# Optimization experiments

Measured on AMD Instinct MI355X. Metric: run time of the kernel, lower is better.

Reference implementation:

```python
import jax, jax.numpy as jnp
import numpy as np

N = 262144      # total atoms (ragged over batch)
B = 64          # batch_size
K = 16          # retrieved features per sample
H = 256         # h_dim
R = 512         # ret_feat_dim


def setup_inputs() -> dict:
    key = jax.random.key(0)
    k1, k2, k3, k4, k5, k6, k7 = jax.random.split(key, 7)
    h = jax.random.normal(k1, (N, H), dtype=jnp.float32)
    ret_feat = jax.random.normal(k2, (B, K, R), dtype=jnp.float32)
    batch = jnp.sort(jax.random.randint(k3, (N,), 0, B, dtype=jnp.int64))
    # nn.Linear weights: y = x @ W.T + b
    Wp = jax.random.normal(k4, (H, R), dtype=jnp.float32) / np.sqrt(R)
    bp = jax.random.normal(k5, (H,), dtype=jnp.float32) * 0.01
    Wl = jax.random.normal(k6, (H, 2 * H), dtype=jnp.float32) / np.sqrt(2 * H)
    bl = jax.random.normal(k7, (H,), dtype=jnp.float32) * 0.01
    return {"h": h, "ret_feat": ret_feat, "batch": batch,
            "Wp": Wp, "bp": bp, "Wl": Wl, "bl": bl}


def reference(h, ret_feat, batch, Wp, bp, Wl, bl):
    # ret_feat: [B, K, R] -> mean over K -> project to [B, H]
    ret = jnp.mean(ret_feat, axis=1)                    # [B, R]
    ret = ret @ Wp.T + bp                               # [B, H]
    # The torch loop gathers h[batch==i], concats the pooled feature
    # repeated per atom, applies `linear`, and scatters back. Since every
    # atom is covered exactly once, this is a per-node gather + linear:
    per_node = ret[batch]                               # [N, H] gather
    x = jnp.concatenate([h, per_node], axis=-1)         # [N, 2H]
    return x @ Wl.T + bl                                # [N, H]
```

## Files before the change

kernel.cpp:

```cpp
#include <hip/hip_runtime.h>
#include <hip/hip_bf16.h>

#define N_ATOMS 262144
#define B_SZ    64
#define H_DIM   256
#define R_DIM   512

#define TILE_ROWS 16
#define TPB       32
#define NBLOCKS   (N_ATOMS / (TILE_ROWS * TPB))
#define NBUF      4

typedef __attribute__((ext_vector_type(8))) short bf16x8;
typedef __attribute__((ext_vector_type(4))) float f32x4;

static __device__ __forceinline__ short f2bf(float f) {
  unsigned u = __builtin_bit_cast(unsigned, f);
  u = (u + 0x7FFFu + ((u >> 16) & 1u)) >> 16;
  return (short)u;
}

static __device__ __forceinline__ unsigned cvtpk(float lo, float hi) {
  unsigned r;
  asm("v_cvt_pk_bf16_f32 %0, %1, %2" : "=v"(r) : "v"(lo), "v"(hi));
  return r;
}

static __device__ __forceinline__ bf16x8 pack8(f32x4 a0, f32x4 a1) {
  unsigned u0 = cvtpk(a0[0], a0[1]);
  unsigned u1 = cvtpk(a0[2], a0[3]);
  unsigned u2 = cvtpk(a1[0], a1[1]);
  unsigned u3 = cvtpk(a1[2], a1[3]);
  bf16x8 v;
  v[0] = (short)(u0 & 0xFFFF); v[1] = (short)(u0 >> 16);
  v[2] = (short)(u1 & 0xFFFF); v[3] = (short)(u1 >> 16);
  v[4] = (short)(u2 & 0xFFFF); v[5] = (short)(u2 >> 16);
  v[6] = (short)(u3 & 0xFFFF); v[7] = (short)(u3 >> 16);
  return v;
}

static __device__ __forceinline__ void async_copy16(const float* g, short* lds) {
  __builtin_amdgcn_global_load_lds(
      (const __attribute__((address_space(1))) unsigned int*)g,
      (__attribute__((address_space(3))) unsigned int*)lds,
      16, 0, 0);
}

__global__ __launch_bounds__(1024) void prep_kernel(
    const float* __restrict__ rf, const float* __restrict__ Wp,
    const float* __restrict__ bp, const float* __restrict__ Wl,
    const float* __restrict__ bl, float* __restrict__ pooled,
    short* __restrict__ Bbf) {
  int t = threadIdx.x;
  if (blockIdx.x >= B_SZ) {
    int base = (blockIdx.x - B_SZ) * 4096 + t * 4;
#pragma unroll
    for (int q = 0; q < 4; ++q) {
      int idx  = base + q;
      int j    = idx & 7;
      int lane = (idx >> 3) & 63;
      int ks   = (idx >> 9) & 7;
      int ct   = idx >> 12;
      int o    = ct * 16 + (lane & 15);
      int k    = ks * 32 + ((lane >> 4) << 3) + j;
      Bbf[idx] = f2bf(Wl[o * (2 * H_DIM) + k]);
    }
    return;
  }

  __shared__ float meanr[R_DIM];
  __shared__ float retj[H_DIM];
  int b    = blockIdx.x;
  int lane = t & 63;
  int w    = t >> 6;

  if (t < R_DIM) {
    float s = 0.f;
    const float* p = rf + (long)b * 16 * R_DIM + t;
#pragma unroll
    for (int k = 0; k < 16; ++k) s += p[k * R_DIM];
    meanr[t] = s * (1.f / 16.f);
  }
  __syncthreads();

  {
    f32x4 m0 = *(const f32x4*)&meanr[lane * 8];
    f32x4 m1 = *(const f32x4*)&meanr[lane * 8 + 4];
#pragma unroll
    for (int jj = 0; jj < 16; ++jj) {
      int j = w * 16 + jj;
      const f32x4* wp = (const f32x4*)(Wp + (long)j * R_DIM + lane * 8);
      f32x4 w0 = wp[0], w1 = wp[1];
      float s = m0[0]*w0[0] + m0[1]*w0[1] + m0[2]*w0[2] + m0[3]*w0[3]
              + m1[0]*w1[0] + m1[1]*w1[1] + m1[2]*w1[2] + m1[3]*w1[3];
#pragma unroll
      for (int d = 1; d < 64; d <<= 1) s += __shfl_xor(s, d);
      if (lane == 0) retj[j] = s + bp[j];
    }
  }
  __syncthreads();

  {
    f32x4 r0 = *(const f32x4*)&retj[lane * 4];
#pragma unroll
    for (int oo = 0; oo < 16; ++oo) {
      int o = w * 16 + oo;
      f32x4 wv = *(const f32x4*)(Wl + (long)o * (2 * H_DIM) + H_DIM + lane * 4);
      float s = r0[0]*wv[0] + r0[1]*wv[1] + r0[2]*wv[2] + r0[3]*wv[3];
#pragma unroll
      for (int d = 1; d < 64; d <<= 1) s += __shfl_xor(s, d);
      if (lane == 0) pooled[b * H_DIM + o] = s + bl[o];
    }
  }
}

__global__ __launch_bounds__(512, 4) void gemm_kernel(
    const float* __restrict__ h, const short* __restrict__ Bbf,
    const float* __restrict__ pooled, const int* __restrict__ batch,
    float* __restrict__ out) {
  __shared__ short As[NBUF][16 * 512];
  int t    = threadIdx.x;
  int lane = t & 63;
  int w    = t >> 6;
  const int arow = lane & 15;
  const int kg   = lane >> 4;

  bf16x8 bfrag0[8], bfrag1[8];
#pragma unroll
  for (int ks = 0; ks < 8; ++ks) {
    bfrag0[ks] = *(const bf16x8*)(Bbf + ((((2 * w)     * 8 + ks) * 64 + lane) << 3));
    bfrag1[ks] = *(const bf16x8*)(Bbf + ((((2 * w + 1) * 8 + ks) * 64 + lane) << 3));
  }

  long base_row = (long)blockIdx.x * (TILE_ROWS * TPB);
  int o0 = (w << 5) + (kg << 2);
  int o1 = o0 + 16;
  const long lsrc = (long)arow * H_DIM + (w << 5) + (kg << 3);

  int b_cur = batch[base_row + arow];
  {
    const float* gp = h + base_row * H_DIM + lsrc;
    async_copy16(gp,     &As[0][(2 * w) * 512]);
    async_copy16(gp + 4, &As[0][(2 * w + 1) * 512]);
  }
  f32x4 pv0, pv1;
  {
    const float* pb = pooled + b_cur * H_DIM;
    pv0 = *(const f32x4*)(pb + o0);
    pv1 = *(const f32x4*)(pb + o1);
  }
  int b_next = batch[base_row + TILE_ROWS + arow];
#pragma unroll
  for (int tl = 1; tl <= 2; ++tl) {
    const float* gp = h + (base_row + (long)tl * TILE_ROWS) * H_DIM + lsrc;
    async_copy16(gp,     &As[tl][(2 * w) * 512]);
    async_copy16(gp + 4, &As[tl][(2 * w + 1) * 512]);
  }
  asm volatile("s_waitcnt vmcnt(4)" ::: "memory");
  __builtin_amdgcn_s_barrier();
  __builtin_amdgcn_sched_barrier(0);

  for (int tt = 0; tt < TPB; ++tt) {
    long g0 = base_row + (long)tt * TILE_ROWS;

    f32x4 npv0 = {0.f, 0.f, 0.f, 0.f}, npv1 = {0.f, 0.f, 0.f, 0.f};
    if (tt + 1 < TPB) {
      const float* pb = pooled + b_next * H_DIM;
      npv0 = *(const f32x4*)(pb + o0);
      npv1 = *(const f32x4*)(pb + o1);
    }
    int b_next2 = 0;
    if (tt + 2 < TPB) b_next2 = batch[g0 + 2 * TILE_ROWS + arow];
    if (tt + 3 < TPB) {
      const float* gp = h + (g0 + 3 * TILE_ROWS) * H_DIM + lsrc;
      short* dst = &As[(tt + 3) & 3][0];
      async_copy16(gp,     dst + (2 * w) * 512);
      async_copy16(gp + 4, dst + (2 * w + 1) * 512);
    }
    __builtin_amdgcn_sched_barrier(0);
    asm volatile("s_waitcnt vmcnt(9)" ::: "memory");
    __builtin_amdgcn_sched_barrier(0);

    const short* ab = &As[tt & 3][0];
    f32x4 acc0 = {0.f, 0.f, 0.f, 0.f};
    f32x4 acc1 = {0.f, 0.f, 0.f, 0.f};
#pragma unroll
    for (int ks = 0; ks < 8; ++ks) {
      f32x4 v0 = *(const f32x4*)(ab + ks * 1024 + lane * 8);
      f32x4 v1 = *(const f32x4*)(ab + ks * 1024 + 512 + lane * 8);
      bf16x8 af = pack8(v0, v1);
      acc0 = __builtin_amdgcn_mfma_f32_16x16x32_bf16(bfrag0[ks], af, acc0, 0, 0, 0);
      acc1 = __builtin_amdgcn_mfma_f32_16x16x32_bf16(bfrag1[ks], af, acc1, 0, 0, 0);
    }
    float* orow = out + (g0 + arow) * H_DIM;
    *(f32x4*)(orow + o0) = acc0 + pv0;
    *(f32x4*)(orow + o1) = acc1 + pv1;

    pv0 = npv0; pv1 = npv1; b_next = b_next2;

    if (tt + 1 < TPB) {
      __builtin_amdgcn_s_barrier();
      __builtin_amdgcn_sched_barrier(0);
    }
  }
}

extern "C" void kernel_launch(void* const* d_in, const int* in_sizes, int n_in,
                              void* d_out, int out_size, void* d_ws, size_t ws_size,
                              hipStream_t stream) {
  const float* h   = (const float*)d_in[0];
  const float* rf  = (const float*)d_in[1];
  const int*   bat = (const int*)d_in[2];
  const float* Wp  = (const float*)d_in[3];
  const float* bp  = (const float*)d_in[4];
  const float* Wl  = (const float*)d_in[5];
  const float* bl  = (const float*)d_in[6];
  float* out = (float*)d_out;

  float* pooled = (float*)d_ws;
  short* Bbf    = (short*)((char*)d_ws + 64 * 1024);

  prep_kernel<<<B_SZ + 16, 1024, 0, stream>>>(rf, Wp, bp, Wl, bl, pooled, Bbf);
  gemm_kernel<<<NBLOCKS, 512, 0, stream>>>(h, Bbf, pooled, bat, out);
}
```

Measured before the change: 146.1 us.

## Stage per-block pooled rows and batch offsets in LDS, uniform async-copy count

Each block loads its 512 batch indices once into LDS as offsets and, when the block spans at most 8 samples, caches those pooled rows in LDS. Per-tile batch and pooled global loads go away. The async copy is now issued every iteration (to a scratch buffer once the tiles run out) so the vmcnt wait stays a constant. Costs are extra LDS, a full vmcnt(0) wait in the prologue, and dummy loads in the last iterations.

```diff
diff --git a/kernel.cpp b/kernel.cpp
--- a/kernel.cpp
+++ b/kernel.cpp
@@ -119,6 +119,9 @@
     const float* __restrict__ pooled, const int* __restrict__ batch,
     float* __restrict__ out) {
   __shared__ short As[NBUF][16 * 512];
+  __shared__ float pooled_lds[8 * 256];
+  __shared__ short boff_lds[512];
+  __shared__ short scratch[512];
   int t    = threadIdx.x;
   int lane = t & 63;
   int w    = t >> 6;
@@ -137,48 +140,52 @@
   int o1 = o0 + 16;
   const long lsrc = (long)arow * H_DIM + (w << 5) + (kg << 3);
 
-  int b_cur = batch[base_row + arow];
-  {
-    const float* gp = h + base_row * H_DIM + lsrc;
-    async_copy16(gp,     &As[0][(2 * w) * 512]);
-    async_copy16(gp + 4, &As[0][(2 * w + 1) * 512]);
-  }
-  f32x4 pv0, pv1;
-  {
-    const float* pb = pooled + b_cur * H_DIM;
-    pv0 = *(const f32x4*)(pb + o0);
-    pv1 = *(const f32x4*)(pb + o1);
-  }
-  int b_next = batch[base_row + TILE_ROWS + arow];
-#pragma unroll
-  for (int tl = 1; tl <= 2; ++tl) {
+  int b_t     = batch[base_row + t];
+  int b_first = batch[base_row];
+  int b_last  = batch[base_row + 511];
+  int span    = b_last - b_first + 1;
+
+#pragma unroll
+  for (int tl = 0; tl < 3; ++tl) {
     const float* gp = h + (base_row + (long)tl * TILE_ROWS) * H_DIM + lsrc;
     async_copy16(gp,     &As[tl][(2 * w) * 512]);
     async_copy16(gp + 4, &As[tl][(2 * w + 1) * 512]);
   }
-  asm volatile("s_waitcnt vmcnt(4)" ::: "memory");
+
+  boff_lds[t] = (short)(b_t - b_first);
+  if (span <= 8) {
+    int fi = t * 4;
+    if (fi < span * H_DIM)
+      *(f32x4*)&pooled_lds[fi] =
+          *(const f32x4*)(pooled + (long)b_first * H_DIM + fi);
+  }
+  asm volatile("s_waitcnt vmcnt(0) lgkmcnt(0)" ::: "memory");
   __builtin_amdgcn_s_barrier();
   __builtin_amdgcn_sched_barrier(0);
 
+  const bool small_span = (span <= 8);
+
   for (int tt = 0; tt < TPB; ++tt) {
     long g0 = base_row + (long)tt * TILE_ROWS;
 
-    f32x4 npv0 = {0.f, 0.f, 0.f, 0.f}, npv1 = {0.f, 0.f, 0.f, 0.f};
-    if (tt + 1 < TPB) {
-      const float* pb = pooled + b_next * H_DIM;
-      npv0 = *(const f32x4*)(pb + o0);
-      npv1 = *(const f32x4*)(pb + o1);
-    }
-    int b_next2 = 0;
-    if (tt + 2 < TPB) b_next2 = batch[g0 + 2 * TILE_ROWS + arow];
-    if (tt + 3 < TPB) {
-      const float* gp = h + (g0 + 3 * TILE_ROWS) * H_DIM + lsrc;
-      short* dst = &As[(tt + 3) & 3][0];
-      async_copy16(gp,     dst + (2 * w) * 512);
-      async_copy16(gp + 4, dst + (2 * w + 1) * 512);
+    {
+      const float* gp;
+      short *d0, *d1;
+      if (tt + 3 < TPB) {
+        gp = h + (g0 + 3 * TILE_ROWS) * H_DIM + lsrc;
+        short* dbuf = &As[(tt + 3) & 3][0];
+        d0 = dbuf + (2 * w) * 512;
+        d1 = dbuf + (2 * w + 1) * 512;
+      } else {
+        gp = h + base_row * H_DIM + lsrc;
+        d0 = scratch;
+        d1 = scratch;
+      }
+      async_copy16(gp,     d0);
+      async_copy16(gp + 4, d1);
     }
     __builtin_amdgcn_sched_barrier(0);
-    asm volatile("s_waitcnt vmcnt(9)" ::: "memory");
+    asm volatile("s_waitcnt vmcnt(10)" ::: "memory");
     __builtin_amdgcn_sched_barrier(0);
 
     const short* ab = &As[tt & 3][0];
@@ -192,16 +199,24 @@
       acc0 = __builtin_amdgcn_mfma_f32_16x16x32_bf16(bfrag0[ks], af, acc0, 0, 0, 0);
       acc1 = __builtin_amdgcn_mfma_f32_16x16x32_bf16(bfrag1[ks], af, acc1, 0, 0, 0);
     }
+
+    int off = (int)boff_lds[tt * 16 + arow];
+    f32x4 pv0, pv1;
+    if (small_span) {
+      pv0 = *(const f32x4*)&pooled_lds[(off << 8) + o0];
+      pv1 = *(const f32x4*)&pooled_lds[(off << 8) + o1];
+    } else {
+      const float* pb = pooled + (long)(b_first + off) * H_DIM;
+      pv0 = *(const f32x4*)(pb + o0);
+      pv1 = *(const f32x4*)(pb + o1);
+    }
+
     float* orow = out + (g0 + arow) * H_DIM;
     *(f32x4*)(orow + o0) = acc0 + pv0;
     *(f32x4*)(orow + o1) = acc1 + pv1;
 
-    pv0 = npv0; pv1 = npv1; b_next = b_next2;
-
-    if (tt + 1 < TPB) {
-      __builtin_amdgcn_s_barrier();
-      __builtin_amdgcn_sched_barrier(0);
-    }
+    __builtin_amdgcn_s_barrier();
+    __builtin_amdgcn_sched_barrier(0);
   }
 }
 
```

Result: no change. 144.8 us (-0.9%).
